# Optimization experiments

Measured on AMD Instinct MI355X. Metric: run time of the kernel, lower is better.

Reference implementation:

```python
import jax, jax.numpy as jnp
from jax import lax
import numpy as np

ORDER = 4        # Butterworth order -> ORDER//2 second-order sections
CUTOFF = 150.0   # Hz
FS = 48000.0     # Hz
B, C, T = 32, 8, 96000


def _butter_lowpass_sos(order: int, cutoff: float, fs: float) -> np.ndarray:
    """Butterworth lowpass design (bilinear transform), SOS output (n_sections, 6).
    Same math as scipy.signal.butter(..., output='sos') up to per-section gain
    distribution (each section normalized to unity DC gain)."""
    assert order % 2 == 0
    warped = 2.0 * fs * np.tan(np.pi * cutoff / fs)  # prewarped analog cutoff
    k = np.arange(order // 2)
    theta = np.pi / 2.0 + np.pi * (2 * k + 1) / (2.0 * order)  # upper-half-plane poles
    p = warped * np.exp(1j * theta)
    fs2 = 2.0 * fs
    z = (fs2 + p) / (fs2 - p)  # bilinear-transformed digital poles
    a1 = -2.0 * z.real
    a2 = np.abs(z) ** 2
    g = (1.0 + a1 + a2) / 4.0  # unity DC gain per section; zeros at z=-1 -> num [1,2,1]
    sos = np.stack([g, 2.0 * g, g, np.ones_like(g), a1, a2], axis=1)
    return sos.astype(np.float32)


def setup_inputs() -> dict:
    key = jax.random.key(0)
    x = jax.random.normal(key, (B, C, T), dtype=jnp.float32)
    sos = jnp.asarray(_butter_lowpass_sos(ORDER, CUTOFF, FS))  # (2, 6)
    return {"x": x, "sos": sos}


def _apply_section(x_nt, b0, b1, b2, a1, a2):
    """Direct Form II biquad over time for all signals in parallel. x_nt: (N, T)."""
    n = x_nt.shape[0]

    def step(carry, x_n):
        w1, w2 = carry
        w0 = x_n - a1 * w1 - a2 * w2
        y_n = b0 * w0 + b1 * w1 + b2 * w2
        return (w0, w1), y_n

    init = (jnp.zeros((n,), x_nt.dtype), jnp.zeros((n,), x_nt.dtype))
    _, y_tn = lax.scan(step, init, x_nt.T)  # scan over T, vectorized over N
    return y_tn.T


def reference(x, sos):
    orig_shape = x.shape
    xf = x.reshape(-1, orig_shape[-1])  # (B*C, T)
    y = xf
    n_sections = sos.shape[0]
    for i in range(n_sections):  # small fixed count (2)
        a0 = sos[i, 3]
        y = _apply_section(
            y,
            sos[i, 0] / a0, sos[i, 1] / a0, sos[i, 2] / a0,
            sos[i, 4] / a0, sos[i, 5] / a0,
        )
    return y.reshape(orig_shape)
```

## Files before the change

kernel.cpp:

```cpp
#include <hip/hip_runtime.h>

#define NSIG   256
#define T_LEN  96000
#define NCHUNK 250
#define CLEN   384

struct Coefs {
  float b01, b11, b21, na11, na21;
  float b02, b12, b22, na12, na22;
};

__device__ __forceinline__ Coefs load_coefs(const float* __restrict__ sos) {
  Coefs c;
  float i0 = 1.0f / sos[3];
  c.b01 = sos[0] * i0; c.b11 = sos[1] * i0; c.b21 = sos[2] * i0;
  c.na11 = -sos[4] * i0; c.na21 = -sos[5] * i0;
  float i1 = 1.0f / sos[9];
  c.b02 = sos[6] * i1; c.b12 = sos[7] * i1; c.b22 = sos[8] * i1;
  c.na12 = -sos[10] * i1; c.na22 = -sos[11] * i1;
  return c;
}

__device__ __forceinline__ float step2(float xin, float& w11, float& w21,
                                       float& w12, float& w22, const Coefs& c) {
  float w0 = fmaf(c.na11, w11, fmaf(c.na21, w21, xin));
  float y1 = fmaf(c.b21, w21, fmaf(c.b11, w11, c.b01 * w0));
  w21 = w11; w11 = w0;
  float w0b = fmaf(c.na12, w12, fmaf(c.na22, w22, y1));
  float y2 = fmaf(c.b22, w22, fmaf(c.b12, w12, c.b02 * w0b));
  w22 = w12; w12 = w0b;
  return y2;
}

__global__ __launch_bounds__(256) void k_phase1(const float* __restrict__ x,
                                                const float* __restrict__ sos,
                                                float4* __restrict__ vzs) {
  int tid = blockIdx.x * 256 + threadIdx.x;
  int sig = tid & (NSIG - 1);
  int chk = tid >> 8;
  Coefs cf = load_coefs(sos);
  const float4* xp = reinterpret_cast<const float4*>(
      x + (size_t)sig * T_LEN + (size_t)chk * CLEN);
  float w11 = 0.f, w21 = 0.f, w12 = 0.f, w22 = 0.f;
#pragma unroll 4
  for (int j = 0; j < CLEN / 4; ++j) {
    float4 xv = xp[j];
    (void)step2(xv.x, w11, w21, w12, w22, cf);
    (void)step2(xv.y, w11, w21, w12, w22, cf);
    (void)step2(xv.z, w11, w21, w12, w22, cf);
    (void)step2(xv.w, w11, w21, w12, w22, cf);
  }
  float4 st; st.x = w11; st.y = w21; st.z = w12; st.w = w22;
  vzs[(size_t)chk * NSIG + sig] = st;
}

__global__ __launch_bounds__(256) void k_scan(const float* __restrict__ sos,
                                              const float4* __restrict__ vzs,
                                              float4* __restrict__ vinit) {
  __shared__ float Ash[16];
  Coefs cf = load_coefs(sos);
  int t = threadIdx.x;
  if (t < 4) {
    float w11 = (t == 0) ? 1.f : 0.f;
    float w21 = (t == 1) ? 1.f : 0.f;
    float w12 = (t == 2) ? 1.f : 0.f;
    float w22 = (t == 3) ? 1.f : 0.f;
    for (int j = 0; j < CLEN; ++j)
      (void)step2(0.f, w11, w21, w12, w22, cf);
    Ash[0 * 4 + t] = w11; Ash[1 * 4 + t] = w21;
    Ash[2 * 4 + t] = w12; Ash[3 * 4 + t] = w22;
  }
  __syncthreads();
  float A[16];
#pragma unroll
  for (int i = 0; i < 16; ++i) A[i] = Ash[i];
  float4 v; v.x = 0.f; v.y = 0.f; v.z = 0.f; v.w = 0.f;
  for (int c = 0; c < NCHUNK; ++c) {
    vinit[(size_t)c * NSIG + t] = v;
    float4 z = vzs[(size_t)c * NSIG + t];
    float4 nv;
    nv.x = fmaf(A[ 3], v.w, fmaf(A[ 2], v.z, fmaf(A[ 1], v.y, fmaf(A[ 0], v.x, z.x))));
    nv.y = fmaf(A[ 7], v.w, fmaf(A[ 6], v.z, fmaf(A[ 5], v.y, fmaf(A[ 4], v.x, z.y))));
    nv.z = fmaf(A[11], v.w, fmaf(A[10], v.z, fmaf(A[ 9], v.y, fmaf(A[ 8], v.x, z.z))));
    nv.w = fmaf(A[15], v.w, fmaf(A[14], v.z, fmaf(A[13], v.y, fmaf(A[12], v.x, z.w))));
    v = nv;
  }
}

__global__ __launch_bounds__(256) void k_phase3(const float* __restrict__ x,
                                                const float* __restrict__ sos,
                                                const float4* __restrict__ vinit,
                                                float* __restrict__ y) {
  int tid = blockIdx.x * 256 + threadIdx.x;
  int sig = tid & (NSIG - 1);
  int chk = tid >> 8;
  Coefs cf = load_coefs(sos);
  size_t base = (size_t)sig * T_LEN + (size_t)chk * CLEN;
  const float4* xp = reinterpret_cast<const float4*>(x + base);
  float4* yp = reinterpret_cast<float4*>(y + base);
  float4 v = vinit[(size_t)chk * NSIG + sig];
  float w11 = v.x, w21 = v.y, w12 = v.z, w22 = v.w;
#pragma unroll 4
  for (int j = 0; j < CLEN / 4; ++j) {
    float4 xv = xp[j];
    float4 yv;
    yv.x = step2(xv.x, w11, w21, w12, w22, cf);
    yv.y = step2(xv.y, w11, w21, w12, w22, cf);
    yv.z = step2(xv.z, w11, w21, w12, w22, cf);
    yv.w = step2(xv.w, w11, w21, w12, w22, cf);
    yp[j] = yv;
  }
}

extern "C" void kernel_launch(void* const* d_in, const int* in_sizes, int n_in,
                              void* d_out, int out_size, void* d_ws, size_t ws_size,
                              hipStream_t stream) {
  const float* x   = (const float*)d_in[0];
  const float* sos = (const float*)d_in[1];
  float* yout = (float*)d_out;
  float4* vzs   = (float4*)d_ws;
  float4* vinit = vzs + (size_t)NCHUNK * NSIG;

  k_phase1<<<NCHUNK, 256, 0, stream>>>(x, sos, vzs);
  k_scan<<<1, 256, 0, stream>>>(sos, vzs, vinit);
  k_phase3<<<NCHUNK, 256, 0, stream>>>(x, sos, vinit, yout);
}
```

Before: 269.0 us.

## Remap phase kernels to one block per signal and prefetch scan loads

Phase 1 and phase 3 now launch one block per signal, with threads indexing chunks, so the 250 active threads of a block walk adjacent chunks of the same signal instead of different signals. The serial k_scan kernel now prefetches its per-chunk state vectors in groups of ten into registers, so the dependent FMA chain is not stalled on each global load. Unroll factors in the phase loops rise from 4 to 8. The trade-offs are 6 idle threads per block, a within-warp access stride of 384 floats instead of 96000, and higher register use in the scan.

New measurement: 241.1 us. 10.4% less time.

```diff
diff --git a/kernel.cpp b/kernel.cpp
--- a/kernel.cpp
+++ b/kernel.cpp
@@ -35,14 +35,14 @@
 __global__ __launch_bounds__(256) void k_phase1(const float* __restrict__ x,
                                                 const float* __restrict__ sos,
                                                 float4* __restrict__ vzs) {
-  int tid = blockIdx.x * 256 + threadIdx.x;
-  int sig = tid & (NSIG - 1);
-  int chk = tid >> 8;
+  int sig = blockIdx.x;
+  int chk = threadIdx.x;
+  if (chk >= NCHUNK) return;
   Coefs cf = load_coefs(sos);
   const float4* xp = reinterpret_cast<const float4*>(
       x + (size_t)sig * T_LEN + (size_t)chk * CLEN);
   float w11 = 0.f, w21 = 0.f, w12 = 0.f, w22 = 0.f;
-#pragma unroll 4
+#pragma unroll 8
   for (int j = 0; j < CLEN / 4; ++j) {
     float4 xv = xp[j];
     (void)step2(xv.x, w11, w21, w12, w22, cf);
@@ -54,6 +54,7 @@
   vzs[(size_t)chk * NSIG + sig] = st;
 }
 
+#define PF 10
 __global__ __launch_bounds__(256) void k_scan(const float* __restrict__ sos,
                                               const float4* __restrict__ vzs,
                                               float4* __restrict__ vinit) {
@@ -74,16 +75,32 @@
   float A[16];
 #pragma unroll
   for (int i = 0; i < 16; ++i) A[i] = Ash[i];
+
+  float4 zb[PF], zb2[PF];
+#pragma unroll
+  for (int i = 0; i < PF; ++i) zb[i] = vzs[(size_t)i * NSIG + t];
   float4 v; v.x = 0.f; v.y = 0.f; v.z = 0.f; v.w = 0.f;
-  for (int c = 0; c < NCHUNK; ++c) {
-    vinit[(size_t)c * NSIG + t] = v;
-    float4 z = vzs[(size_t)c * NSIG + t];
-    float4 nv;
-    nv.x = fmaf(A[ 3], v.w, fmaf(A[ 2], v.z, fmaf(A[ 1], v.y, fmaf(A[ 0], v.x, z.x))));
-    nv.y = fmaf(A[ 7], v.w, fmaf(A[ 6], v.z, fmaf(A[ 5], v.y, fmaf(A[ 4], v.x, z.y))));
-    nv.z = fmaf(A[11], v.w, fmaf(A[10], v.z, fmaf(A[ 9], v.y, fmaf(A[ 8], v.x, z.z))));
-    nv.w = fmaf(A[15], v.w, fmaf(A[14], v.z, fmaf(A[13], v.y, fmaf(A[12], v.x, z.w))));
-    v = nv;
+  for (int g = 0; g < NCHUNK / PF; ++g) {
+#pragma unroll
+    for (int i = 0; i < PF; ++i) {
+      int c2 = (g + 1) * PF + i;
+      c2 = c2 < NCHUNK ? c2 : NCHUNK - 1;
+      zb2[i] = vzs[(size_t)c2 * NSIG + t];
+    }
+#pragma unroll
+    for (int i = 0; i < PF; ++i) {
+      int c = g * PF + i;
+      vinit[(size_t)c * NSIG + t] = v;
+      float4 z = zb[i];
+      float4 nv;
+      nv.x = fmaf(A[ 3], v.w, fmaf(A[ 2], v.z, fmaf(A[ 1], v.y, fmaf(A[ 0], v.x, z.x))));
+      nv.y = fmaf(A[ 7], v.w, fmaf(A[ 6], v.z, fmaf(A[ 5], v.y, fmaf(A[ 4], v.x, z.y))));
+      nv.z = fmaf(A[11], v.w, fmaf(A[10], v.z, fmaf(A[ 9], v.y, fmaf(A[ 8], v.x, z.z))));
+      nv.w = fmaf(A[15], v.w, fmaf(A[14], v.z, fmaf(A[13], v.y, fmaf(A[12], v.x, z.w))));
+      v = nv;
+    }
+#pragma unroll
+    for (int i = 0; i < PF; ++i) zb[i] = zb2[i];
   }
 }
 
@@ -91,16 +108,16 @@
                                                 const float* __restrict__ sos,
                                                 const float4* __restrict__ vinit,
                                                 float* __restrict__ y) {
-  int tid = blockIdx.x * 256 + threadIdx.x;
-  int sig = tid & (NSIG - 1);
-  int chk = tid >> 8;
+  int sig = blockIdx.x;
+  int chk = threadIdx.x;
+  if (chk >= NCHUNK) return;
   Coefs cf = load_coefs(sos);
   size_t base = (size_t)sig * T_LEN + (size_t)chk * CLEN;
   const float4* xp = reinterpret_cast<const float4*>(x + base);
   float4* yp = reinterpret_cast<float4*>(y + base);
   float4 v = vinit[(size_t)chk * NSIG + sig];
   float w11 = v.x, w21 = v.y, w12 = v.z, w22 = v.w;
-#pragma unroll 4
+#pragma unroll 8
   for (int j = 0; j < CLEN / 4; ++j) {
     float4 xv = xp[j];
     float4 yv;
@@ -121,7 +138,7 @@
   float4* vzs   = (float4*)d_ws;
   float4* vinit = vzs + (size_t)NCHUNK * NSIG;
 
-  k_phase1<<<NCHUNK, 256, 0, stream>>>(x, sos, vzs);
+  k_phase1<<<NSIG, 256, 0, stream>>>(x, sos, vzs);
   k_scan<<<1, 256, 0, stream>>>(sos, vzs, vinit);
-  k_phase3<<<NCHUNK, 256, 0, stream>>>(x, sos, vinit, yout);
+  k_phase3<<<NSIG, 256, 0, stream>>>(x, sos, vinit, yout);
 }
```
